# Kernel optimization log

Measured on AMD Instinct MI355X. Metric: run time of the kernel, lower is better.

Reference implementation:

```python
import jax, jax.numpy as jnp
import numpy as np

N, E, D_IN, HID, HEADS, D_OUT, R = 20000, 640000, 256, 128, 4, 128, 32
NEG_SLOPE = 0.2  # PyG GATConv default


def setup_inputs() -> dict:
    key = jax.random.key(0)
    ks = jax.random.split(key, 12)
    s = 0.05
    return {
        "x": jax.random.normal(ks[0], (N, D_IN), jnp.float32),
        "edge_index": jax.random.randint(ks[1], (2, E), 0, N, dtype=jnp.int64),
        "edge_type": jax.random.randint(ks[2], (E,), 0, R, dtype=jnp.int64),
        "rel_emb": jax.random.normal(ks[3], (R, D_IN), jnp.float32) * s,
        "W1": jax.random.normal(ks[4], (D_IN, HEADS * HID), jnp.float32) * s,
        "att_src1": jax.random.normal(ks[5], (HEADS, HID), jnp.float32) * s,
        "att_dst1": jax.random.normal(ks[6], (HEADS, HID), jnp.float32) * s,
        "b1": jnp.zeros((HEADS * HID,), jnp.float32),
        "W2": jax.random.normal(ks[7], (HEADS * HID, D_OUT), jnp.float32) * s,
        "att_src2": jax.random.normal(ks[8], (1, D_OUT), jnp.float32) * s,
        "att_dst2": jax.random.normal(ks[9], (1, D_OUT), jnp.float32) * s,
        "b2": jnp.zeros((D_OUT,), jnp.float32),
    }


def _gat_conv(x, src, dst, W, a_src, a_dst, bias, heads, ch):
    """PyG GATConv (eval mode, self loops already in src/dst)."""
    n = x.shape[0]
    h = (x @ W).reshape(n, heads, ch)                      # [N,H,C]
    alpha_s = jnp.einsum('nhc,hc->nh', h, a_src)           # [N,H]
    alpha_d = jnp.einsum('nhc,hc->nh', h, a_dst)
    e = jax.nn.leaky_relu(alpha_s[src] + alpha_d[dst], NEG_SLOPE)  # [E,H]
    # segment softmax over incoming edges of each dst node
    m = jax.ops.segment_max(e, dst, num_segments=n)        # [N,H]
    p = jnp.exp(e - m[dst])
    denom = jax.ops.segment_sum(p, dst, num_segments=n)
    alpha = p / (denom[dst] + 1e-16)                       # [E,H]
    out = jax.ops.segment_sum(h[src] * alpha[:, :, None], dst, num_segments=n)
    return out.reshape(n, heads * ch) + bias


def reference(x, edge_index, edge_type, rel_emb, W1, att_src1, att_dst1, b1,
              W2, att_src2, att_dst2, b2):
    src, dst = edge_index[0], edge_index[1]
    # relational feature injection: x_mod[src] += rel_emb[edge_type]
    x_mod = x.at[src].add(rel_emb[edge_type])
    # GATConv adds self loops by default
    loop = jnp.arange(N, dtype=src.dtype)
    s2 = jnp.concatenate([src, loop])
    d2 = jnp.concatenate([dst, loop])
    h = _gat_conv(x_mod, s2, d2, W1, att_src1, att_dst1, b1, HEADS, HID)
    h = jax.nn.elu(h)
    return _gat_conv(h, s2, d2, W2, att_src2, att_dst2, b2, 1, D_OUT)
```

## Files before the change

### kernel.cpp

```cpp
#include <hip/hip_runtime.h>


#define D_IN   256
#define HID1   512
#define NHEADS 4
#define DOUT   128
#define NREL   32
#define NEG_SLOPE 0.2f
#define M_PAD  20096
#define NB     128

static __device__ __forceinline__ unsigned short f2b(float f) {
  union { float f; unsigned int i; } v; v.f = f;
  unsigned int x = v.i;
  return (unsigned short)((x + 0x7fffu + ((x >> 16) & 1u)) >> 16);
}
static __device__ __forceinline__ float lrelu(float x) {
  return x > 0.f ? x : NEG_SLOPE * x;
}

typedef __attribute__((ext_vector_type(8))) short bf16x8;
typedef __attribute__((ext_vector_type(4))) float f32x4;
typedef __attribute__((ext_vector_type(2))) float f32x2;

static __device__ __forceinline__ f32x2 up2(unsigned int u) {
  union { unsigned int i; float f; } lo, hi;
  lo.i = u << 16; hi.i = u & 0xffff0000u;
  f32x2 v; v.x = lo.f; v.y = hi.f; return v;
}
static __device__ __forceinline__ void pkfma(f32x2& a, f32x2 b, f32x2 c) {
  asm("v_pk_fma_f32 %0, %1, %2, %0" : "+v"(a) : "v"(b), "v"(c));
}
static __device__ __forceinline__ void pkfma_l(f32x2& a, f32x2 b, f32x2 c) {
  asm("v_pk_fma_f32 %0, %1, %2, %0 op_sel_hi:[0,1,1]"
      : "+v"(a) : "v"(b), "v"(c));
}
static __device__ __forceinline__ void pkfma_h(f32x2& a, f32x2 b, f32x2 c) {
  asm("v_pk_fma_f32 %0, %1, %2, %0 op_sel:[1,0,0]"
      : "+v"(a) : "v"(b), "v"(c));
}
static __device__ __forceinline__ void accp(f32x2* acc, float w, uint4 r) {
  f32x2 wv = (f32x2)(w);
  pkfma(acc[0], wv, up2(r.x));
  pkfma(acc[1], wv, up2(r.y));
  pkfma(acc[2], wv, up2(r.z));
  pkfma(acc[3], wv, up2(r.w));
}
static __device__ __forceinline__ void acc4w(f32x2 acc[4][4], f32x2& den01,
                                             f32x2& den23, float4 w, uint4 r) {
  f32x2 w01; w01.x = w.x; w01.y = w.y;
  f32x2 w23; w23.x = w.z; w23.y = w.w;
  den01 += w01; den23 += w23;
  f32x2 x0 = up2(r.x), x1 = up2(r.y), x2 = up2(r.z), x3 = up2(r.w);
  pkfma_l(acc[0][0], w01, x0); pkfma_l(acc[0][1], w01, x1);
  pkfma_l(acc[0][2], w01, x2); pkfma_l(acc[0][3], w01, x3);
  pkfma_h(acc[1][0], w01, x0); pkfma_h(acc[1][1], w01, x1);
  pkfma_h(acc[1][2], w01, x2); pkfma_h(acc[1][3], w01, x3);
  pkfma_l(acc[2][0], w23, x0); pkfma_l(acc[2][1], w23, x1);
  pkfma_l(acc[2][2], w23, x2); pkfma_l(acc[2][3], w23, x3);
  pkfma_h(acc[3][0], w23, x0); pkfma_h(acc[3][1], w23, x1);
  pkfma_h(acc[3][2], w23, x2); pkfma_h(acc[3][3], w23, x3);
}

__global__ __launch_bounds__(256) void hist_prep_kernel(
    const int* __restrict__ src, const int* __restrict__ dst,
    const int* __restrict__ et, unsigned int* __restrict__ counts8,
    int* __restrict__ gtable, int E, int n, int cb,
    const float* __restrict__ W1, const float* __restrict__ W2,
    unsigned short* __restrict__ W1T, unsigned short* __restrict__ W2T,
    const float* __restrict__ att_s1, const float* __restrict__ att_d1,
    float* __restrict__ us4, float* __restrict__ ud4,
    const float* __restrict__ att_s2, const float* __restrict__ att_d2,
    float* __restrict__ vs, float* __restrict__ vd) {
  int b = blockIdx.x;
  int t = threadIdx.x;
  if (b < NB) {
    extern __shared__ int hist[];
    for (int i = t; i < n; i += 256) hist[i] = 0;
    __syncthreads();
    int per = (E + NB - 1) / NB;
    int e0 = b * per;
    int e1 = min(e0 + per, E);
    for (int e = e0 + t; e < e1; e += 256) {
      atomicAdd(&hist[dst[e]], 1);
      int s = src[e], r = et[e];
      atomicAdd(&counts8[(size_t)s * 8 + (r >> 2)], 1u << (8 * (r & 3)));
    }
    __syncthreads();
    for (int i = t; i < n; i += 256) gtable[(size_t)b * n + i] = hist[i];
  } else if (b < NB + cb) {
    int idx = (b - NB) * 256 + t;
    if (idx < D_IN * HID1) {
      int r = idx / HID1, c = idx % HID1;
      W1T[(size_t)c * D_IN + r] = f2b(W1[idx]);
    } else {
      int k = idx - D_IN * HID1;
      if (k < HID1 * DOUT) {
        int r = k / DOUT, c = k % DOUT;
        W2T[(size_t)c * HID1 + r] = f2b(W2[k]);
      }
    }
  } else if (b < NB + cb + 8) {
    int k = (b - NB - cb) * 32 + (t >> 3);
    int ch0 = (t & 7) * 64;
    int h = (t & 7) >> 1;
    const float4* w4 = (const float4*)(W1 + (size_t)k * HID1 + ch0);
    const float4* s4 = (const float4*)(att_s1 + ch0);
    const float4* d4 = (const float4*)(att_d1 + ch0);
    float us = 0.f, ud = 0.f;
#pragma unroll
    for (int i = 0; i < 16; ++i) {
      float4 wv = w4[i], sv = s4[i], dv = d4[i];
      us += wv.x * sv.x + wv.y * sv.y + wv.z * sv.z + wv.w * sv.w;
      ud += wv.x * dv.x + wv.y * dv.y + wv.z * dv.z + wv.w * dv.w;
    }
    us += __shfl_xor(us, 1);
    ud += __shfl_xor(ud, 1);
    if ((t & 1) == 0) { us4[k * 4 + h] = us; ud4[k * 4 + h] = ud; }
  } else {
    int r = (b - NB - cb - 8) * 128 + (t >> 1);
    int c0 = (t & 1) * 64;
    const float4* w4 = (const float4*)(W2 + (size_t)r * DOUT + c0);
    const float4* s4 = (const float4*)(att_s2 + c0);
    const float4* d4 = (const float4*)(att_d2 + c0);
    float ss = 0.f, dd = 0.f;
#pragma unroll
    for (int i = 0; i < 16; ++i) {
      float4 wv = w4[i], sv = s4[i], dv = d4[i];
      ss += wv.x * sv.x + wv.y * sv.y + wv.z * sv.z + wv.w * sv.w;
      dd += wv.x * dv.x + wv.y * dv.y + wv.z * dv.z + wv.w * dv.w;
    }
    ss += __shfl_xor(ss, 1);
    dd += __shfl_xor(dd, 1);
    if ((t & 1) == 0) { vs[r] = ss; vd[r] = dd; }
  }
}

__global__ __launch_bounds__(256) void colsum_xmod_kernel(
    const int* __restrict__ gtable, int* __restrict__ offsets, int cs,
    const float* __restrict__ x, const unsigned int* __restrict__ counts8,
    const float* __restrict__ rel, const float* __restrict__ us4,
    const float* __restrict__ ud4, unsigned short* __restrict__ x_modb,
    float* __restrict__ as1, float* __restrict__ ad1, int n_nodes) {
  int b = blockIdx.x;
  int t = threadIdx.x;
  if (b < cs) {
    int d = b * 256 + t;
    if (d >= n_nodes) return;
    int s = 0;
    for (int bb = 0; bb < NB; ++bb) s += gtable[(size_t)bb * n_nodes + d];
    offsets[d] = s;
    return;
  }
  int wv = t >> 6;
  int node = (b - cs) * 4 + wv;
  if (node >= n_nodes) return;
  int l = t & 63;
  int r5 = l & 31;
  unsigned int cw = counts8[(size_t)node * 8 + (r5 >> 2)];
  int cnt_l = (int)((cw >> (8 * (r5 & 3))) & 0xffu);
  const float4* x4 = (const float4*)x;
  const float4* rel4 = (const float4*)rel;
  float4 v = x4[(size_t)node * 64 + l];
#pragma unroll
  for (int r = 0; r < NREL; ++r) {
    int c = __shfl(cnt_l, r);
    if (c) {
      float4 rv = rel4[r * 64 + l];
      float fc = (float)c;
      v.x += fc * rv.x; v.y += fc * rv.y; v.z += fc * rv.z; v.w += fc * rv.w;
    }
  }
  ushort4 o;
  o.x = f2b(v.x); o.y = f2b(v.y); o.z = f2b(v.z); o.w = f2b(v.w);
  *(ushort4*)(x_modb + (size_t)node * D_IN + l * 4) = o;
  const float4* usv = (const float4*)us4;
  const float4* udv = (const float4*)ud4;
  float vv[4] = {v.x, v.y, v.z, v.w};
  float sh[4] = {0.f, 0.f, 0.f, 0.f}, dh[4] = {0.f, 0.f, 0.f, 0.f};
#pragma unroll
  for (int i = 0; i < 4; ++i) {
    float4 uu = usv[l * 4 + i];
    float4 dd = udv[l * 4 + i];
    sh[0] += vv[i] * uu.x; sh[1] += vv[i] * uu.y; sh[2] += vv[i] * uu.z; sh[3] += vv[i] * uu.w;
    dh[0] += vv[i] * dd.x; dh[1] += vv[i] * dd.y; dh[2] += vv[i] * dd.z; dh[3] += vv[i] * dd.w;
  }
  for (int off = 32; off; off >>= 1) {
#pragma unroll
    for (int h = 0; h < 4; ++h) {
      sh[h] += __shfl_xor(sh[h], off);
      dh[h] += __shfl_xor(dh[h], off);
    }
  }
  if (l == 0) {
    ((float4*)as1)[node] = make_float4(sh[0], sh[1], sh[2], sh[3]);
    ((float4*)ad1)[node] = make_float4(dh[0], dh[1], dh[2], dh[3]);
  }
}

__global__ __launch_bounds__(256) void scan_full_kernel(int* __restrict__ offsets,
                                                        int n) {
  __shared__ int wsum[4];
  __shared__ int carry;
  int t = threadIdx.x;
  int lane = t & 63, w = t >> 6;
  if (t == 0) carry = 0;
  __syncthreads();
  for (int base = 0; base < n; base += 256) {
    int i = base + t;
    int v = (i < n) ? offsets[i] : 0;
    int sc = v;
    for (int off = 1; off < 64; off <<= 1) {
      int u = __shfl_up(sc, off);
      if (lane >= off) sc += u;
    }
    if (lane == 63) wsum[w] = sc;
    __syncthreads();
    int woff = carry;
    for (int k = 0; k < w; ++k) woff += wsum[k];
    if (i < n) offsets[i] = woff + sc - v;
    __syncthreads();
    if (t == 255) carry = woff + sc;
    __syncthreads();
  }
  if (t == 0) offsets[n] = carry;
}

__global__ void rebase_kernel(int* __restrict__ gtable,
                              const int* __restrict__ offsets, int n) {
  int d = blockIdx.x * 256 + threadIdx.x;
  if (d >= n) return;
  int run = offsets[d];
  for (int b = 0; b < NB; ++b) {
    size_t idx = (size_t)b * n + d;
    int v = gtable[idx];
    gtable[idx] = run;
    run += v;
  }
}

__global__ __launch_bounds__(256) void scatter2_kernel(
    const int* __restrict__ src, const int* __restrict__ dst,
    const int* __restrict__ gtable, int* __restrict__ csr_src,
    float4* __restrict__ wexp,
    const float* __restrict__ as1, const float* __restrict__ ad1,
    int E, int n) {
  extern __shared__ int cur[];
  int b = blockIdx.x;
  int t = threadIdx.x;
  for (int i = t; i < n; i += 256) cur[i] = gtable[(size_t)b * n + i];
  __syncthreads();
  int per = (E + NB - 1) / NB;
  int e0 = b * per;
  int e1 = min(e0 + per, E);
  for (int e = e0 + t; e < e1; e += 256) {
    int d = dst[e], s = src[e];
    int pos = atomicAdd(&cur[d], 1);
    csr_src[pos] = s;
    float4 av = ((const float4*)as1)[s];
    float4 dv = ((const float4*)ad1)[d];
    wexp[pos] = make_float4(__expf(lrelu(av.x + dv.x)),
                            __expf(lrelu(av.y + dv.y)),
                            __expf(lrelu(av.z + dv.z)),
                            __expf(lrelu(av.w + dv.w)));
  }
}

__global__ __launch_bounds__(256) void aggregate1_kernel(
    const unsigned short* __restrict__ x_modb,
    const float4* __restrict__ wexp,
    const float* __restrict__ as1, const float* __restrict__ ad1,
    const int* __restrict__ offsets, const int* __restrict__ csr_src,
    unsigned short* __restrict__ agg_xb, int n_nodes) {
  int node = blockIdx.x * 4 + (threadIdx.x >> 6);
  if (node >= n_nodes) return;
  int lane = threadIdx.x & 63;
  int half = lane >> 5, l32 = lane & 31;
  int lo = offsets[node], hi = offsets[node + 1];
  const uint4* xv = (const uint4*)x_modb;
  const float4 z4 = make_float4(0.f, 0.f, 0.f, 0.f);

  f32x2 acc[4][4];
#pragma unroll
  for (int h = 0; h < 4; ++h)
#pragma unroll
    for (int k = 0; k < 4; ++k) acc[h][k] = (f32x2)(0.f);
  f32x2 den01 = (f32x2)(0.f), den23 = (f32x2)(0.f);

  int j = lo + half;
  int s0 = (j < hi) ? csr_src[j] : node;
  float4 wA = (j < hi) ? wexp[j] : z4;
  uint4 rA = xv[(unsigned)((s0 << 5) | l32)];
  int j1 = j + 2;
  int s1 = (j1 < hi) ? csr_src[j1] : node;
  float4 wB = (j1 < hi) ? wexp[j1] : z4;
  uint4 rB = xv[(unsigned)((s1 << 5) | l32)];
  while (j < hi) {
    int jA = j + 4;
    int sA = (jA < hi) ? csr_src[jA] : node;
    float4 wAn = (jA < hi) ? wexp[jA] : z4;
    uint4 rAn = xv[(unsigned)((sA << 5) | l32)];
    acc4w(acc, den01, den23, wA, rA);
    int jB = j + 6;
    int sB = (jB < hi) ? csr_src[jB] : node;
    float4 wBn = (jB < hi) ? wexp[jB] : z4;
    uint4 rBn = xv[(unsigned)((sB << 5) | l32)];
    acc4w(acc, den01, den23, wB, rB);
    j = jA; wA = wAn; rA = rAn; wB = wBn; rB = rBn;
  }
  if (half == 0) {
    float4 av = ((const float4*)as1)[node];
    float4 dv = ((const float4*)ad1)[node];
    float4 sw = make_float4(__expf(lrelu(av.x + dv.x)),
                            __expf(lrelu(av.y + dv.y)),
                            __expf(lrelu(av.z + dv.z)),
                            __expf(lrelu(av.w + dv.w)));
    uint4 rs = xv[(unsigned)((node << 5) | l32)];
    acc4w(acc, den01, den23, sw, rs);
  }
#pragma unroll
  for (int h = 0; h < 4; ++h)
#pragma unroll
    for (int k = 0; k < 4; ++k) {
      acc[h][k].x += __shfl_xor(acc[h][k].x, 32);
      acc[h][k].y += __shfl_xor(acc[h][k].y, 32);
    }
  den01.x += __shfl_xor(den01.x, 32); den01.y += __shfl_xor(den01.y, 32);
  den23.x += __shfl_xor(den23.x, 32); den23.y += __shfl_xor(den23.y, 32);
  if (half == 0) {
    float inv[4];
    inv[0] = 1.f / (den01.x + 1e-16f);
    inv[1] = 1.f / (den01.y + 1e-16f);
    inv[2] = 1.f / (den23.x + 1e-16f);
    inv[3] = 1.f / (den23.y + 1e-16f);
#pragma unroll
    for (int h = 0; h < 4; ++h) {
      uint4 o;
      o.x = (unsigned)f2b(acc[h][0].x * inv[h]) | ((unsigned)f2b(acc[h][0].y * inv[h]) << 16);
      o.y = (unsigned)f2b(acc[h][1].x * inv[h]) | ((unsigned)f2b(acc[h][1].y * inv[h]) << 16);
      o.z = (unsigned)f2b(acc[h][2].x * inv[h]) | ((unsigned)f2b(acc[h][2].y * inv[h]) << 16);
      o.w = (unsigned)f2b(acc[h][3].x * inv[h]) | ((unsigned)f2b(acc[h][3].y * inv[h]) << 16);
      *(uint4*)(agg_xb + ((size_t)h * M_PAD + node) * D_IN + l32 * 8) = o;
    }
  }
}

template <int BM, int MODE>
__global__ __launch_bounds__(256) void mfma_gemm(
    const unsigned short* __restrict__ A, const unsigned short* __restrict__ BT,
    unsigned short* __restrict__ C, int M, int N, int K,
    const float* __restrict__ bias, const float* __restrict__ vs,
    const float* __restrict__ vd, float* __restrict__ as2, float* __restrict__ ad2) {
  constexpr int MFR = BM / 32;
  __shared__ __align__(16) unsigned short Asl[BM * 32];
  __shared__ __align__(16) unsigned short Bsl[128 * 32];
  int tid = threadIdx.x;
  int m0 = blockIdx.y * BM, n0 = blockIdx.x * 128;
  int lane = tid & 63, wv = tid >> 6;
  int wm = wv & 1, wn = wv >> 1;
  int l16 = lane & 15, quad = lane >> 4;
  int lr = lane >> 2, lseg = lane & 3;
  if (MODE == 1) A += (size_t)blockIdx.x * M_PAD * K;

  f32x4 acc[MFR][4];
#pragma unroll
  for (int i = 0; i < MFR; ++i)
#pragma unroll
    for (int j = 0; j < 4; ++j) acc[i][j] = (f32x4)(0.f);

  for (int k0 = 0; k0 < K; k0 += 32) {
#pragma unroll
    for (int c = wv; c < BM / 16; c += 4) {
      int gr = m0 + c * 16 + lr; gr = gr < M ? gr : M - 1;
      __builtin_amdgcn_global_load_lds(
          (const __attribute__((address_space(1))) void*)(A + (size_t)gr * K + k0 + lseg * 8),
          (__attribute__((address_space(3))) void*)(&Asl[c * 512]), 16, 0, 0);
    }
#pragma unroll
    for (int c = wv; c < 8; c += 4) {
      int gr = n0 + c * 16 + lr;
      __builtin_amdgcn_global_load_lds(
          (const __attribute__((address_space(1))) void*)(BT + (size_t)gr * K + k0 + lseg * 8),
          (__attribute__((address_space(3))) void*)(&Bsl[c * 512]), 16, 0, 0);
    }
    __syncthreads();
    bf16x8 af[MFR], bfr[4];
#pragma unroll
    for (int mf = 0; mf < MFR; ++mf)
      af[mf] = *(const bf16x8*)(&Asl[(wm * (BM / 2) + mf * 16 + l16) * 32 + quad * 8]);
#pragma unroll
    for (int nf = 0; nf < 4; ++nf)
      bfr[nf] = *(const bf16x8*)(&Bsl[(wn * 64 + nf * 16 + l16) * 32 + quad * 8]);
#pragma unroll
    for (int mf = 0; mf < MFR; ++mf)
#pragma unroll
      for (int nf = 0; nf < 4; ++nf)
        acc[mf][nf] = __builtin_amdgcn_mfma_f32_16x16x32_bf16(af[mf], bfr[nf], acc[mf][nf], 0, 0, 0);
    __syncthreads();
  }
  if (MODE == 0) {
#pragma unroll
    for (int mf = 0; mf < MFR; ++mf)
#pragma unroll
      for (int nf = 0; nf < 4; ++nf)
#pragma unroll
        for (int r = 0; r < 4; ++r) {
          int row = m0 + wm * (BM / 2) + mf * 16 + quad * 4 + r;
          int col = n0 + wn * 64 + nf * 16 + l16;
          C[(size_t)row * N + col] = f2b(acc[mf][nf][r]);
        }
  } else {
#pragma unroll
    for (int mf = 0; mf < MFR; ++mf)
#pragma unroll
      for (int r = 0; r < 4; ++r) {
        int row = m0 + wm * (BM / 2) + mf * 16 + quad * 4 + r;
        float sd = 0.f, dd = 0.f;
#pragma unroll
        for (int nf = 0; nf < 4; ++nf) {
          int col = n0 + wn * 64 + nf * 16 + l16;
          float cv = acc[mf][nf][r] + bias[col];
          cv = cv > 0.f ? cv : expm1f(cv);
          C[(size_t)row * N + col] = f2b(cv);
          sd += cv * vs[col];
          dd += cv * vd[col];
        }
#pragma unroll
        for (int off = 1; off < 16; off <<= 1) {
          sd += __shfl_xor(sd, off);
          dd += __shfl_xor(dd, off);
        }
        if (l16 == 0 && row < M) {
          atomicAdd(&as2[row], sd);
          atomicAdd(&ad2[row], dd);
        }
      }
  }
}

__global__ __launch_bounds__(256) void aggregate2_kernel(
    const unsigned short* __restrict__ t2b,
    const float* __restrict__ as2, const float* __restrict__ ad2,
    const int* __restrict__ offsets, const int* __restrict__ csr_src,
    const float* __restrict__ bias, float* __restrict__ out, int n_nodes) {
  int node = blockIdx.x * 4 + (threadIdx.x >> 6);
  if (node >= n_nodes) return;
  int lane = threadIdx.x & 63;
  int g = lane >> 4, l16 = lane & 15;
  int lo = offsets[node], hi = offsets[node + 1];
  float ad = ad2[node];

  const uint4* t2v = (const uint4*)t2b;
  f32x2 acc[4];
#pragma unroll
  for (int k = 0; k < 4; ++k) acc[k] = (f32x2)(0.f);
  float denom = 0.f;
  int nit = (hi - lo + 3) >> 2;
  int j = lo + g;
  bool valid = j < hi;
  int s = valid ? csr_src[j] : node;
  float asv = as2[s];
  uint4 tv = t2v[(unsigned)((s << 4) | l16)];
  for (int i = 0; i < nit; ++i) {
    int jn = j + 4;
    bool vn = jn < hi;
    int sn = vn ? csr_src[jn] : node;
    float asv_n = as2[sn];
    uint4 tvn = t2v[(unsigned)((sn << 4) | l16)];
    float w = valid ? __expf(lrelu(asv + ad)) : 0.f;
    accp(acc, w, tv);
    denom += w;
    j = jn; valid = vn; s = sn; asv = asv_n; tv = tvn;
  }
  if (g == 0) {
    uint4 tv2 = t2v[(unsigned)((node << 4) | l16)];
    float w = __expf(lrelu(as2[node] + ad));
    accp(acc, w, tv2);
    denom += w;
  }
#pragma unroll
  for (int k = 0; k < 4; ++k) {
    acc[k].x += __shfl_xor(acc[k].x, 16); acc[k].y += __shfl_xor(acc[k].y, 16);
    acc[k].x += __shfl_xor(acc[k].x, 32); acc[k].y += __shfl_xor(acc[k].y, 32);
  }
  denom += __shfl_xor(denom, 16);
  denom += __shfl_xor(denom, 32);
  if (g == 0) {
    float inv = 1.f / (denom + 1e-16f);
    float4 o0, o1;
    o0.x = acc[0].x * inv + bias[l16 * 8 + 0];
    o0.y = acc[0].y * inv + bias[l16 * 8 + 1];
    o0.z = acc[1].x * inv + bias[l16 * 8 + 2];
    o0.w = acc[1].y * inv + bias[l16 * 8 + 3];
    o1.x = acc[2].x * inv + bias[l16 * 8 + 4];
    o1.y = acc[2].y * inv + bias[l16 * 8 + 5];
    o1.z = acc[3].x * inv + bias[l16 * 8 + 6];
    o1.w = acc[3].y * inv + bias[l16 * 8 + 7];
    *(float4*)(out + (size_t)node * DOUT + l16 * 8) = o0;
    *(float4*)(out + (size_t)node * DOUT + l16 * 8 + 4) = o1;
  }
}

extern "C" void kernel_launch(void* const* d_in, const int* in_sizes, int n_in,
                              void* d_out, int out_size, void* d_ws, size_t ws_size,
                              hipStream_t stream) {
  const float* x     = (const float*)d_in[0];
  const int* ei      = (const int*)d_in[1];
  const int* etype   = (const int*)d_in[2];
  const float* rel   = (const float*)d_in[3];
  const float* W1    = (const float*)d_in[4];
  const float* at_s1 = (const float*)d_in[5];
  const float* at_d1 = (const float*)d_in[6];
  const float* b1    = (const float*)d_in[7];
  const float* W2    = (const float*)d_in[8];
  const float* at_s2 = (const float*)d_in[9];
  const float* at_d2 = (const float*)d_in[10];
  const float* b2v   = (const float*)d_in[11];
  float* out         = (float*)d_out;

  const int N = in_sizes[0] / D_IN;
  const int E = in_sizes[2];
  const int* srcv = ei;
  const int* dstv = ei + E;

  char* p = (char*)d_ws;
  auto carve = [&](size_t bytes) -> char* {
    char* r = p; p += (bytes + 255) & ~(size_t)255; return r;
  };
  unsigned int* counts8 = (unsigned int*)carve((size_t)N * 8 * 4);
  float* as2     = (float*)carve((size_t)N * 4);
  float* ad2     = (float*)carve((size_t)N * 4);
  size_t zero_bytes = (size_t)(p - (char*)counts8);
  int*   offsets = (int*)carve(((size_t)N + 1) * 4);
  float* as1     = (float*)carve((size_t)N * NHEADS * 4);
  float* ad1     = (float*)carve((size_t)N * NHEADS * 4);
  float* vs      = (float*)carve((size_t)HID1 * 4);
  float* vd      = (float*)carve((size_t)HID1 * 4);
  float* us4     = (float*)carve((size_t)D_IN * 4 * 4);
  float* ud4     = (float*)carve((size_t)D_IN * 4 * 4);
  int*   csr_src = (int*)carve((size_t)E * 4);
  float4* wexp   = (float4*)carve((size_t)E * 16);
  unsigned short* W1T    = (unsigned short*)carve((size_t)HID1 * D_IN * 2);
  unsigned short* W2T    = (unsigned short*)carve((size_t)DOUT * HID1 * 2);
  unsigned short* x_modb = (unsigned short*)carve((size_t)N * D_IN * 2);
  unsigned short* agg_xb = (unsigned short*)carve((size_t)NHEADS * M_PAD * D_IN * 2);
  unsigned short* h2b    = (unsigned short*)carve((size_t)M_PAD * HID1 * 2);
  unsigned short* t2b    = (unsigned short*)carve((size_t)M_PAD * DOUT * 2);
  int* gtable = (int*)h2b;

  (void)hipMemsetAsync(counts8, 0, zero_bytes, stream);

  int cb = (D_IN * HID1 + HID1 * DOUT + 255) / 256;
  int cs = (N + 255) / 256;
  int xb = (N + 3) / 4;
  int ldsb = N * 4;
  hist_prep_kernel<<<NB + cb + 12, 256, ldsb, stream>>>(
      srcv, dstv, etype, counts8, gtable, E, N, cb,
      W1, W2, W1T, W2T, at_s1, at_d1, us4, ud4, at_s2, at_d2, vs, vd);
  colsum_xmod_kernel<<<cs + xb, 256, 0, stream>>>(
      gtable, offsets, cs, x, counts8, rel, us4, ud4, x_modb, as1, ad1, N);
  scan_full_kernel<<<1, 256, 0, stream>>>(offsets, N);
  rebase_kernel<<<cs, 256, 0, stream>>>(gtable, offsets, N);
  scatter2_kernel<<<NB, 256, ldsb, stream>>>(srcv, dstv, gtable, csr_src, wexp,
                                             as1, ad1, E, N);
  aggregate1_kernel<<<xb, 256, 0, stream>>>(x_modb, wexp, as1, ad1, offsets,
                                            csr_src, agg_xb, N);
  mfma_gemm<128, 1><<<dim3(NHEADS, M_PAD / 128), 256, 0, stream>>>(
      agg_xb, W1T, h2b, N, HID1, D_IN, b1, vs, vd, as2, ad2);
  mfma_gemm<64, 0><<<dim3(DOUT / 128, M_PAD / 64), 256, 0, stream>>>(
      h2b, W2T, t2b, N, DOUT, HID1, nullptr, nullptr, nullptr, nullptr, nullptr);
  aggregate2_kernel<<<xb, 256, 0, stream>>>(
      t2b, as2, ad2, offsets, csr_src, b2v, out, N);
}
```

Measured before the change: 363.4 us.

## Store edge attention weights as bf16 and parallelize the CSR offset scan

```diff
diff --git a/kernel.cpp b/kernel.cpp
--- a/kernel.cpp
+++ b/kernel.cpp
@@ -46,10 +46,9 @@
   pkfma(acc[2], wv, up2(r.z));
   pkfma(acc[3], wv, up2(r.w));
 }
-static __device__ __forceinline__ void acc4w(f32x2 acc[4][4], f32x2& den01,
-                                             f32x2& den23, float4 w, uint4 r) {
-  f32x2 w01; w01.x = w.x; w01.y = w.y;
-  f32x2 w23; w23.x = w.z; w23.y = w.w;
+static __device__ __forceinline__ void acc4wb(f32x2 acc[4][4], f32x2& den01,
+                                              f32x2& den23, uint2 w, uint4 r) {
+  f32x2 w01 = up2(w.x), w23 = up2(w.y);
   den01 += w01; den23 += w23;
   f32x2 x0 = up2(r.x), x1 = up2(r.y), x2 = up2(r.z), x3 = up2(r.w);
   pkfma_l(acc[0][0], w01, x0); pkfma_l(acc[0][1], w01, x1);
@@ -198,32 +197,51 @@
   }
 }
 
-__global__ __launch_bounds__(256) void scan_full_kernel(int* __restrict__ offsets,
-                                                        int n) {
+__global__ void scan_local(int* __restrict__ data, int* __restrict__ bsum,
+                           int n) {
   __shared__ int wsum[4];
-  __shared__ int carry;
   int t = threadIdx.x;
+  int base = blockIdx.x * 1024 + t * 4;
+  int v0 = (base + 0 < n) ? data[base + 0] : 0;
+  int v1 = (base + 1 < n) ? data[base + 1] : 0;
+  int v2 = (base + 2 < n) ? data[base + 2] : 0;
+  int v3 = (base + 3 < n) ? data[base + 3] : 0;
+  int s = v0 + v1 + v2 + v3;
   int lane = t & 63, w = t >> 6;
-  if (t == 0) carry = 0;
+  int sc = s;
+  for (int off = 1; off < 64; off <<= 1) {
+    int u = __shfl_up(sc, off);
+    if (lane >= off) sc += u;
+  }
+  if (lane == 63) wsum[w] = sc;
   __syncthreads();
-  for (int base = 0; base < n; base += 256) {
-    int i = base + t;
-    int v = (i < n) ? offsets[i] : 0;
-    int sc = v;
-    for (int off = 1; off < 64; off <<= 1) {
-      int u = __shfl_up(sc, off);
-      if (lane >= off) sc += u;
-    }
-    if (lane == 63) wsum[w] = sc;
-    __syncthreads();
-    int woff = carry;
-    for (int k = 0; k < w; ++k) woff += wsum[k];
-    if (i < n) offsets[i] = woff + sc - v;
-    __syncthreads();
-    if (t == 255) carry = woff + sc;
-    __syncthreads();
-  }
-  if (t == 0) offsets[n] = carry;
+  int woff = 0;
+  for (int i = 0; i < w; ++i) woff += wsum[i];
+  int excl = woff + sc - s;
+  if (base + 0 < n) data[base + 0] = excl;
+  if (base + 1 < n) data[base + 1] = excl + v0;
+  if (base + 2 < n) data[base + 2] = excl + v0 + v1;
+  if (base + 3 < n) data[base + 3] = excl + v0 + v1 + v2;
+  if (t == 255) bsum[blockIdx.x] = woff + sc;
+}
+
+__global__ void scan_blocks(int* __restrict__ bsum, int nb,
+                            int* __restrict__ offsets, int n) {
+  int t = threadIdx.x;
+  int v = (t < nb) ? bsum[t] : 0;
+  int sc = v;
+  for (int off = 1; off < 64; off <<= 1) {
+    int u = __shfl_up(sc, off);
+    if (t >= off) sc += u;
+  }
+  if (t < nb) bsum[t] = sc - v;
+  if (t == nb - 1) offsets[n] = v;
+}
+
+__global__ void fixup_kernel(int* __restrict__ offsets,
+                             const int* __restrict__ bsum, int n) {
+  int i = blockIdx.x * 256 + threadIdx.x;
+  if (i <= n) offsets[i] += bsum[i >> 10];
 }
 
 __global__ void rebase_kernel(int* __restrict__ gtable,
@@ -242,7 +260,7 @@
 __global__ __launch_bounds__(256) void scatter2_kernel(
     const int* __restrict__ src, const int* __restrict__ dst,
     const int* __restrict__ gtable, int* __restrict__ csr_src,
-    float4* __restrict__ wexp,
+    uint2* __restrict__ wexp,
     const float* __restrict__ as1, const float* __restrict__ ad1,
     int E, int n) {
   extern __shared__ int cur[];
@@ -259,16 +277,18 @@
     csr_src[pos] = s;
     float4 av = ((const float4*)as1)[s];
     float4 dv = ((const float4*)ad1)[d];
-    wexp[pos] = make_float4(__expf(lrelu(av.x + dv.x)),
-                            __expf(lrelu(av.y + dv.y)),
-                            __expf(lrelu(av.z + dv.z)),
-                            __expf(lrelu(av.w + dv.w)));
+    unsigned short h0 = f2b(__expf(lrelu(av.x + dv.x)));
+    unsigned short h1 = f2b(__expf(lrelu(av.y + dv.y)));
+    unsigned short h2 = f2b(__expf(lrelu(av.z + dv.z)));
+    unsigned short h3 = f2b(__expf(lrelu(av.w + dv.w)));
+    wexp[pos] = make_uint2((unsigned)h0 | ((unsigned)h1 << 16),
+                           (unsigned)h2 | ((unsigned)h3 << 16));
   }
 }
 
 __global__ __launch_bounds__(256) void aggregate1_kernel(
     const unsigned short* __restrict__ x_modb,
-    const float4* __restrict__ wexp,
+    const uint2* __restrict__ wexp,
     const float* __restrict__ as1, const float* __restrict__ ad1,
     const int* __restrict__ offsets, const int* __restrict__ csr_src,
     unsigned short* __restrict__ agg_xb, int n_nodes) {
@@ -278,7 +298,7 @@
   int half = lane >> 5, l32 = lane & 31;
   int lo = offsets[node], hi = offsets[node + 1];
   const uint4* xv = (const uint4*)x_modb;
-  const float4 z4 = make_float4(0.f, 0.f, 0.f, 0.f);
+  const uint2 z2 = make_uint2(0u, 0u);
 
   f32x2 acc[4][4];
 #pragma unroll
@@ -289,34 +309,36 @@
 
   int j = lo + half;
   int s0 = (j < hi) ? csr_src[j] : node;
-  float4 wA = (j < hi) ? wexp[j] : z4;
+  uint2 wA = (j < hi) ? wexp[j] : z2;
   uint4 rA = xv[(unsigned)((s0 << 5) | l32)];
   int j1 = j + 2;
   int s1 = (j1 < hi) ? csr_src[j1] : node;
-  float4 wB = (j1 < hi) ? wexp[j1] : z4;
+  uint2 wB = (j1 < hi) ? wexp[j1] : z2;
   uint4 rB = xv[(unsigned)((s1 << 5) | l32)];
   while (j < hi) {
     int jA = j + 4;
     int sA = (jA < hi) ? csr_src[jA] : node;
-    float4 wAn = (jA < hi) ? wexp[jA] : z4;
+    uint2 wAn = (jA < hi) ? wexp[jA] : z2;
     uint4 rAn = xv[(unsigned)((sA << 5) | l32)];
-    acc4w(acc, den01, den23, wA, rA);
+    acc4wb(acc, den01, den23, wA, rA);
     int jB = j + 6;
     int sB = (jB < hi) ? csr_src[jB] : node;
-    float4 wBn = (jB < hi) ? wexp[jB] : z4;
+    uint2 wBn = (jB < hi) ? wexp[jB] : z2;
     uint4 rBn = xv[(unsigned)((sB << 5) | l32)];
-    acc4w(acc, den01, den23, wB, rB);
+    acc4wb(acc, den01, den23, wB, rB);
     j = jA; wA = wAn; rA = rAn; wB = wBn; rB = rBn;
   }
   if (half == 0) {
     float4 av = ((const float4*)as1)[node];
     float4 dv = ((const float4*)ad1)[node];
-    float4 sw = make_float4(__expf(lrelu(av.x + dv.x)),
-                            __expf(lrelu(av.y + dv.y)),
-                            __expf(lrelu(av.z + dv.z)),
-                            __expf(lrelu(av.w + dv.w)));
+    unsigned short h0 = f2b(__expf(lrelu(av.x + dv.x)));
+    unsigned short h1 = f2b(__expf(lrelu(av.y + dv.y)));
+    unsigned short h2 = f2b(__expf(lrelu(av.z + dv.z)));
+    unsigned short h3 = f2b(__expf(lrelu(av.w + dv.w)));
+    uint2 sw = make_uint2((unsigned)h0 | ((unsigned)h1 << 16),
+                          (unsigned)h2 | ((unsigned)h3 << 16));
     uint4 rs = xv[(unsigned)((node << 5) | l32)];
-    acc4w(acc, den01, den23, sw, rs);
+    acc4wb(acc, den01, den23, sw, rs);
   }
 #pragma unroll
   for (int h = 0; h < 4; ++h)
@@ -532,6 +554,7 @@
   float* ad2     = (float*)carve((size_t)N * 4);
   size_t zero_bytes = (size_t)(p - (char*)counts8);
   int*   offsets = (int*)carve(((size_t)N + 1) * 4);
+  int*   bsum    = (int*)carve(64 * 4);
   float* as1     = (float*)carve((size_t)N * NHEADS * 4);
   float* ad1     = (float*)carve((size_t)N * NHEADS * 4);
   float* vs      = (float*)carve((size_t)HID1 * 4);
@@ -539,7 +562,7 @@
   float* us4     = (float*)carve((size_t)D_IN * 4 * 4);
   float* ud4     = (float*)carve((size_t)D_IN * 4 * 4);
   int*   csr_src = (int*)carve((size_t)E * 4);
-  float4* wexp   = (float4*)carve((size_t)E * 16);
+  uint2* wexp    = (uint2*)carve((size_t)E * 8);
   unsigned short* W1T    = (unsigned short*)carve((size_t)HID1 * D_IN * 2);
   unsigned short* W2T    = (unsigned short*)carve((size_t)DOUT * HID1 * 2);
   unsigned short* x_modb = (unsigned short*)carve((size_t)N * D_IN * 2);
@@ -553,13 +576,16 @@
   int cb = (D_IN * HID1 + HID1 * DOUT + 255) / 256;
   int cs = (N + 255) / 256;
   int xb = (N + 3) / 4;
+  int nb = (N + 1023) / 1024;
   int ldsb = N * 4;
   hist_prep_kernel<<<NB + cb + 12, 256, ldsb, stream>>>(
       srcv, dstv, etype, counts8, gtable, E, N, cb,
       W1, W2, W1T, W2T, at_s1, at_d1, us4, ud4, at_s2, at_d2, vs, vd);
   colsum_xmod_kernel<<<cs + xb, 256, 0, stream>>>(
       gtable, offsets, cs, x, counts8, rel, us4, ud4, x_modb, as1, ad1, N);
-  scan_full_kernel<<<1, 256, 0, stream>>>(offsets, N);
+  scan_local<<<nb, 256, 0, stream>>>(offsets, bsum, N);
+  scan_blocks<<<1, 64, 0, stream>>>(bsum, nb, offsets, N);
+  fixup_kernel<<<(N + 256) / 256, 256, 0, stream>>>(offsets, bsum, N);
   rebase_kernel<<<cs, 256, 0, stream>>>(gtable, offsets, N);
   scatter2_kernel<<<NB, 256, ldsb, stream>>>(srcv, dstv, gtable, csr_src, wexp,
                                              as1, ad1, E, N);
```

Result: faster. 312.3 us (-14.1%).
